# Performance work log

Hardware: AMD Instinct MI355X
Metric: run time of the kernel (lower is better)

Reference implementation:

```python
import jax, jax.numpy as jnp
import numpy as np

N, D, C = 4096, 1024, 10000
NUM_USED_CLASSES = 1000  # targets drawn from a subset so positives exist per row


def setup_inputs() -> dict:
    key = jax.random.key(0)
    k1, k2, k3 = jax.random.split(key, 3)
    inputs = jax.random.normal(k1, (N, D), dtype=jnp.float32)
    targets = jax.random.randint(k2, (N,), 0, NUM_USED_CLASSES, dtype=jnp.int64)
    w = jax.random.normal(k3, (C, D), dtype=jnp.float32)
    return {"inputs": inputs, "targets": targets, "w": w}


def reference(inputs, targets, w):
    # w_ = w[targets] : per-sample class proxy rows, shape [n, d]
    w_ = w[targets]
    # sim_mat[i, j] = <inputs[i], w[targets[j]]>, shape [n, n]
    sim = jnp.einsum('id,jd->ij', inputs, w_)
    # pos_mask[i, j] = (targets[i] == targets[j]); diagonal is always True,
    # so every row has >= 1 positive. neg_mask is the complement.
    pos = (targets[:, None] == targets[None, :]).astype(sim.dtype)
    neg = 1.0 - pos
    pos_cnt = pos.sum(axis=1)            # >= 1 (diagonal)
    neg_cnt = neg.sum(axis=1)            # >= 1 for n > count of any class
    # Per row: mean over positives of (1 - sim) + mean over negatives of sim.
    # (The sort in the original is a no-op before taking the mean.)
    pos_loss = ((1.0 - sim) * pos).sum(axis=1) / pos_cnt
    neg_loss = (sim * neg).sum(axis=1) / neg_cnt
    return jnp.mean(pos_loss + neg_loss)
```

## Files before the change

kernel.cpp:

```cpp
#include <hip/hip_runtime.h>

#define WAVE 64
#define NCHUNK 64
#define K2_WAVES 8
#define K2_THREADS (K2_WAVES * WAVE)

__global__ __launch_bounds__(256)
void sgather_kernel(const float* __restrict__ w, const int* __restrict__ targets,
                    int N, int D, float* __restrict__ S_part,
                    int* __restrict__ flag) {
    if (blockIdx.x == 0 && threadIdx.x == 0) *flag = 0;
    __shared__ int t_lds[512];
    const int chunk = blockIdx.x;
    const int rows_per = (N + gridDim.x - 1) / gridDim.x;
    const int r0 = chunk * rows_per;
    const int r1 = min(r0 + rows_per, N);
    const int nrows = min(r1 - r0, 512);
    for (int i = threadIdx.x; i < nrows; i += blockDim.x)
        t_lds[i] = targets[r0 + i];
    __syncthreads();
    const int ncol4 = D >> 2;
    for (int d4 = threadIdx.x; d4 < ncol4; d4 += blockDim.x) {
        float ax = 0.f, ay = 0.f, az = 0.f, aw = 0.f;
        #pragma unroll 8
        for (int i = 0; i < nrows; ++i) {
            float4 v = ((const float4*)(w + (size_t)t_lds[i] * D))[d4];
            ax += v.x; ay += v.y; az += v.z; aw += v.w;
        }
        ((float4*)(S_part + (size_t)chunk * D))[d4] = make_float4(ax, ay, az, aw);
    }
}

__global__ __launch_bounds__(K2_THREADS)
void row_kernel(const float* __restrict__ x, const int* __restrict__ targets,
                const float* __restrict__ w, const float* __restrict__ S_part,
                int N, int D,
                float* __restrict__ partials, int* __restrict__ flag,
                float* __restrict__ out) {
    __shared__ float S_lds[4096];
    __shared__ float sm[K2_WAVES];
    __shared__ double dm[K2_WAVES];
    __shared__ int s_old;
    const int tid = threadIdx.x;
    const int ncol4 = D >> 2;

    for (int d4 = tid; d4 < ncol4; d4 += K2_THREADS) {
        float ax = 0.f, ay = 0.f, az = 0.f, aw = 0.f;
        #pragma unroll 8
        for (int c2 = 0; c2 < NCHUNK; ++c2) {
            float4 v = ((const float4*)(S_part + (size_t)c2 * D))[d4];
            ax += v.x; ay += v.y; az += v.z; aw += v.w;
        }
        ((float4*)S_lds)[d4] = make_float4(ax, ay, az, aw);
    }

    const int wave = tid >> 6, lane = tid & 63;
    const int row = blockIdx.x * K2_WAVES + wave;

    int t = 0, c = 0;
    if (row < N) {
        t = targets[row];
        #pragma unroll 8
        for (int j = lane; j < N; j += WAVE) c += (targets[j] == t) ? 1 : 0;
    }

    __syncthreads();

    float term = 0.f;
    if (row < N) {
        const float4* xr = (const float4*)(x + (size_t)row * D);
        const float4* wr = (const float4*)(w + (size_t)t * D);
        const float4* Sr = (const float4*)S_lds;
        float dw = 0.f, ds = 0.f;
        #pragma unroll 4
        for (int k = lane; k < ncol4; k += WAVE) {
            float4 a = xr[k], b = wr[k], s = Sr[k];
            dw += a.x*b.x + a.y*b.y + a.z*b.z + a.w*b.w;
            ds += a.x*s.x + a.y*s.y + a.z*s.z + a.w*s.w;
        }
        #pragma unroll
        for (int off = 32; off; off >>= 1) {
            dw += __shfl_down(dw, off);
            ds += __shfl_down(ds, off);
            c  += __shfl_down(c,  off);
        }
        if (lane == 0) {
            float cf = (float)c;
            term = 1.f - dw + (ds - cf * dw) / ((float)N - cf);
        }
    }
    if (lane == 0) sm[wave] = term;
    __syncthreads();

    if (tid == 0) {
        float p = 0.f;
        #pragma unroll
        for (int i = 0; i < K2_WAVES; ++i) p += sm[i];
        partials[blockIdx.x] = p;
        __threadfence();
        s_old = atomicAdd(flag, 1);
    }
    __syncthreads();
    if (s_old == (int)gridDim.x - 1) {
        __threadfence();
        double acc = 0.0;
        for (int i = tid; i < (int)gridDim.x; i += K2_THREADS) acc += (double)partials[i];
        #pragma unroll
        for (int off = 32; off; off >>= 1) acc += __shfl_down(acc, off);
        if (lane == 0) dm[wave] = acc;
        __syncthreads();
        if (tid == 0) {
            double s2 = 0.0;
            #pragma unroll
            for (int i = 0; i < K2_WAVES; ++i) s2 += dm[i];
            out[0] = (float)(s2 / (double)N);
        }
    }
}

extern "C" void kernel_launch(void* const* d_in, const int* in_sizes, int n_in,
                              void* d_out, int out_size, void* d_ws, size_t ws_size,
                              hipStream_t stream) {
    const float* x       = (const float*)d_in[0];
    const int*   targets = (const int*)d_in[1];
    const float* w       = (const float*)d_in[2];

    int N = in_sizes[1];
    int D = in_sizes[0] / N;

    int nblocks = (N + K2_WAVES - 1) / K2_WAVES;

    char* wsb = (char*)d_ws;
    size_t sp_bytes = ((size_t)NCHUNK * D * sizeof(float) + 255) & ~(size_t)255;
    size_t p_bytes  = ((size_t)nblocks * sizeof(float) + 255) & ~(size_t)255;
    float* S_part   = (float*)wsb;
    float* partials = (float*)(wsb + sp_bytes);
    int*   flag     = (int*)(wsb + sp_bytes + p_bytes);

    sgather_kernel<<<NCHUNK, 256, 0, stream>>>(w, targets, N, D, S_part, flag);
    row_kernel<<<nblocks, K2_THREADS, 0, stream>>>(x, targets, w, S_part, N, D,
                                                   partials, flag, (float*)d_out);
}
```

Before: 38.40 us.

## Reduce gathered partial sums once in separate kernel instead of per block

Adds a small kernel that sums the per-chunk partial column sums of the gathered weight rows into a single vector S in global memory. The row kernel then reads S directly instead of every one of its 512 blocks re-reducing all 64 partial rows into LDS. This removes redundant global reads and an LDS staging step, and lets the row kernel drop a block barrier and its 16KB LDS allocation. The cost is an extra kernel launch and S being read from global/L2 rather than LDS.

```diff
diff --git a/kernel.cpp b/kernel.cpp
--- a/kernel.cpp
+++ b/kernel.cpp
@@ -8,14 +8,13 @@
 __global__ __launch_bounds__(256)
 void sgather_kernel(const float* __restrict__ w, const int* __restrict__ targets,
                     int N, int D, float* __restrict__ S_part,
-                    int* __restrict__ flag) {
-    if (blockIdx.x == 0 && threadIdx.x == 0) *flag = 0;
+                    int* __restrict__ flagB) {
+    if (blockIdx.x == 0 && threadIdx.x == 0) *flagB = 0;
     __shared__ int t_lds[512];
     const int chunk = blockIdx.x;
-    const int rows_per = (N + gridDim.x - 1) / gridDim.x;
+    const int rows_per = (N + NCHUNK - 1) / NCHUNK;
     const int r0 = chunk * rows_per;
-    const int r1 = min(r0 + rows_per, N);
-    const int nrows = min(r1 - r0, 512);
+    const int nrows = min(min(rows_per, N - r0), 512);
     for (int i = threadIdx.x; i < nrows; i += blockDim.x)
         t_lds[i] = targets[r0 + i];
     __syncthreads();
@@ -31,46 +30,44 @@
     }
 }
 
+__global__ __launch_bounds__(64)
+void sreduce_kernel(const float* __restrict__ S_part, int D, float* __restrict__ S) {
+    const int d4 = blockIdx.x * 64 + threadIdx.x;
+    const int ncol4 = D >> 2;
+    if (d4 >= ncol4) return;
+    float ax = 0.f, ay = 0.f, az = 0.f, aw = 0.f;
+    #pragma unroll 8
+    for (int c2 = 0; c2 < NCHUNK; ++c2) {
+        float4 v = ((const float4*)(S_part + (size_t)c2 * D))[d4];
+        ax += v.x; ay += v.y; az += v.z; aw += v.w;
+    }
+    ((float4*)S)[d4] = make_float4(ax, ay, az, aw);
+}
+
 __global__ __launch_bounds__(K2_THREADS)
 void row_kernel(const float* __restrict__ x, const int* __restrict__ targets,
-                const float* __restrict__ w, const float* __restrict__ S_part,
+                const float* __restrict__ w, const float* __restrict__ S,
                 int N, int D,
-                float* __restrict__ partials, int* __restrict__ flag,
+                float* __restrict__ partials, int* __restrict__ flagB,
                 float* __restrict__ out) {
-    __shared__ float S_lds[4096];
     __shared__ float sm[K2_WAVES];
     __shared__ double dm[K2_WAVES];
     __shared__ int s_old;
     const int tid = threadIdx.x;
-    const int ncol4 = D >> 2;
-
-    for (int d4 = tid; d4 < ncol4; d4 += K2_THREADS) {
-        float ax = 0.f, ay = 0.f, az = 0.f, aw = 0.f;
-        #pragma unroll 8
-        for (int c2 = 0; c2 < NCHUNK; ++c2) {
-            float4 v = ((const float4*)(S_part + (size_t)c2 * D))[d4];
-            ax += v.x; ay += v.y; az += v.z; aw += v.w;
-        }
-        ((float4*)S_lds)[d4] = make_float4(ax, ay, az, aw);
-    }
-
     const int wave = tid >> 6, lane = tid & 63;
     const int row = blockIdx.x * K2_WAVES + wave;
-
-    int t = 0, c = 0;
-    if (row < N) {
-        t = targets[row];
-        #pragma unroll 8
-        for (int j = lane; j < N; j += WAVE) c += (targets[j] == t) ? 1 : 0;
-    }
-
-    __syncthreads();
+    const int ncol4 = D >> 2;
 
     float term = 0.f;
     if (row < N) {
+        const int t = targets[row];
+        int c = 0;
+        #pragma unroll 8
+        for (int j = lane; j < N; j += WAVE) c += (targets[j] == t) ? 1 : 0;
+
         const float4* xr = (const float4*)(x + (size_t)row * D);
         const float4* wr = (const float4*)(w + (size_t)t * D);
-        const float4* Sr = (const float4*)S_lds;
+        const float4* Sr = (const float4*)S;
         float dw = 0.f, ds = 0.f;
         #pragma unroll 4
         for (int k = lane; k < ncol4; k += WAVE) {
@@ -98,7 +95,7 @@
         for (int i = 0; i < K2_WAVES; ++i) p += sm[i];
         partials[blockIdx.x] = p;
         __threadfence();
-        s_old = atomicAdd(flag, 1);
+        s_old = atomicAdd(flagB, 1);
     }
     __syncthreads();
     if (s_old == (int)gridDim.x - 1) {
@@ -129,15 +126,19 @@
     int D = in_sizes[0] / N;
 
     int nblocks = (N + K2_WAVES - 1) / K2_WAVES;
+    int ncol4 = D >> 2;
 
     char* wsb = (char*)d_ws;
     size_t sp_bytes = ((size_t)NCHUNK * D * sizeof(float) + 255) & ~(size_t)255;
+    size_t s_bytes  = ((size_t)D * sizeof(float) + 255) & ~(size_t)255;
     size_t p_bytes  = ((size_t)nblocks * sizeof(float) + 255) & ~(size_t)255;
     float* S_part   = (float*)wsb;
-    float* partials = (float*)(wsb + sp_bytes);
-    int*   flag     = (int*)(wsb + sp_bytes + p_bytes);
+    float* S        = (float*)(wsb + sp_bytes);
+    float* partials = (float*)(wsb + sp_bytes + s_bytes);
+    int*   flagB    = (int*)(wsb + sp_bytes + s_bytes + p_bytes);
 
-    sgather_kernel<<<NCHUNK, 256, 0, stream>>>(w, targets, N, D, S_part, flag);
-    row_kernel<<<nblocks, K2_THREADS, 0, stream>>>(x, targets, w, S_part, N, D,
-                                                   partials, flag, (float*)d_out);
+    sgather_kernel<<<NCHUNK, 256, 0, stream>>>(w, targets, N, D, S_part, flagB);
+    sreduce_kernel<<<(ncol4 + 63) / 64, 64, 0, stream>>>(S_part, D, S);
+    row_kernel<<<nblocks, K2_THREADS, 0, stream>>>(x, targets, w, S, N, D,
+                                                   partials, flagB, (float*)d_out);
 }
```

Result: faster. 36.82 us (-4.1%).
